# Performance work log

Hardware: AMD Instinct MI355X
Metric: run time of the kernel (lower is better)

Reference implementation:

```python
import jax, jax.numpy as jnp
import numpy as np

N_NODES = 100000
N_EDGES = 1600000
IN_FEA = 128
HIDDEN = 128
OUT_FEA = 40


def setup_inputs() -> dict:
    key = jax.random.key(0)
    k1, k2, k3, k4 = jax.random.split(key, 4)
    x = jax.random.normal(k1, (N_NODES, IN_FEA), dtype=jnp.float32)
    edge_index = jax.random.randint(k2, (2, N_EDGES), 0, N_NODES, dtype=jnp.int32)
    # Glorot-ish scaled weights
    W1 = jax.random.normal(k3, (IN_FEA, HIDDEN), dtype=jnp.float32) * (1.0 / np.sqrt(IN_FEA))
    b1 = jnp.zeros((HIDDEN,), dtype=jnp.float32)
    W2 = jax.random.normal(k4, (HIDDEN, OUT_FEA), dtype=jnp.float32) * (1.0 / np.sqrt(HIDDEN))
    b2 = jnp.zeros((OUT_FEA,), dtype=jnp.float32)
    return {"x": x, "edge_index": edge_index, "W1": W1, "b1": b1, "W2": W2, "b2": b2}


def _gcn_conv(x, src, dst, norm, W, b, n_nodes):
    # Linear transform first (PyG GCNConv order), then normalized scatter-add.
    h = x @ W                                   # [N, H]
    msg = h[src] * norm[:, None]                # [E+N, H] gather + scale
    out = jax.ops.segment_sum(msg, dst, num_segments=n_nodes)
    return out + b


def reference(x, edge_index, W1, b1, W2, b2):
    n = x.shape[0]
    loops = jnp.arange(n, dtype=edge_index.dtype)
    src = jnp.concatenate([edge_index[0], loops])  # add self-loops
    dst = jnp.concatenate([edge_index[1], loops])
    # Symmetric degree normalization: deg computed at destination (col)
    deg = jax.ops.segment_sum(jnp.ones_like(dst, dtype=x.dtype), dst, num_segments=n)
    dinv = jax.lax.rsqrt(jnp.maximum(deg, 1.0))
    norm = dinv[src] * dinv[dst]                # [E+N]

    h = jax.nn.relu(_gcn_conv(x, src, dst, norm, W1, b1, n))
    # dropout is identity in eval mode
    logits = _gcn_conv(h, src, dst, norm, W2, b2, n)
    return jax.nn.log_softmax(logits, axis=1)
```

## Files before the change

kernel.cpp:

```cpp
#include <hip/hip_runtime.h>
#include <math.h>

#define N_NODES 100000
#define N_EDGES 1600000
#define CHUNK 4096
#define NCH ((N_EDGES + CHUNK - 1) / CHUNK)
#define DSH 9
#define NBD ((N_NODES + 511) / 512)
#define CAP 9216
#define RCAP 10240

typedef __attribute__((ext_vector_type(8))) short bf16x8;
typedef __attribute__((ext_vector_type(4))) float f32x4;
typedef __attribute__((ext_vector_type(2))) float f32x2;

union U4S8 { uint4 u; bf16x8 s; };

__device__ inline unsigned pk_bf16(float a, float b) {
    unsigned ua = __float_as_uint(a), ub = __float_as_uint(b);
    ua = (ua + 0x7FFFu + ((ua >> 16) & 1u)) >> 16;
    ub = (ub + 0x7FFFu + ((ub >> 16) & 1u)) >> 16;
    return (ua & 0xFFFFu) | (ub << 16);
}
__device__ inline unsigned short bf16_1(float a) {
    unsigned ua = __float_as_uint(a);
    return (unsigned short)((ua + 0x7FFFu + ((ua >> 16) & 1u)) >> 16);
}
__device__ inline float bf_lo(unsigned u) { return __uint_as_float(u << 16); }
__device__ inline float bf_hi(unsigned u) { return __uint_as_float(u & 0xFFFF0000u); }

__device__ inline bf16x8 load_cvt8(const float* p) {
    float4 f0 = *(const float4*)p;
    float4 f1 = *(const float4*)(p + 4);
    U4S8 r;
    r.u = make_uint4(pk_bf16(f0.x, f0.y), pk_bf16(f0.z, f0.w),
                     pk_bf16(f1.x, f1.y), pk_bf16(f1.z, f1.w));
    return r.s;
}

__device__ inline void acc8_fp8(f32x2* a, uint2 v) {
    a[0] += __builtin_amdgcn_cvt_pk_f32_fp8((int)v.x, false);
    a[1] += __builtin_amdgcn_cvt_pk_f32_fp8((int)v.x, true);
    a[2] += __builtin_amdgcn_cvt_pk_f32_fp8((int)v.y, false);
    a[3] += __builtin_amdgcn_cvt_pk_f32_fp8((int)v.y, true);
}


__global__ __launch_bounds__(256) void k_prep(const float* __restrict__ W1, const float* __restrict__ W2,
                                              unsigned* __restrict__ W1t, unsigned* __restrict__ W2t,
                                              unsigned* __restrict__ Hb, unsigned* __restrict__ H2b) {
    __shared__ short L[16384];
    int t = threadIdx.x;
    if (blockIdx.x == 0) {
        for (int i = t; i < 16384; i += 256) {
            int k = i >> 7, n = i & 127;
            L[n * 128 + k] = (short)bf16_1(W1[i]);
        }
        __syncthreads();
        uint4* out = (uint4*)W1t;
        const uint4* src = (const uint4*)L;
        for (int i = t; i < 2048; i += 256) out[i] = src[i];
        if (t < 32) Hb[(size_t)N_NODES * 32 + t] = 0u;
    } else {
        for (int i = t; i < 48 * 128; i += 256) L[i] = 0;
        __syncthreads();
        for (int i = t; i < 5120; i += 256) {
            int k = i / 40, n = i - k * 40;
            L[n * 128 + k] = (short)bf16_1(W2[i]);
        }
        __syncthreads();
        uint4* out = (uint4*)W2t;
        const uint4* src = (const uint4*)L;
        for (int i = t; i < 768; i += 256) out[i] = src[i];
        if (t < 10) H2b[(size_t)N_NODES * 10 + t] = 0u;
    }
}


__global__ __launch_bounds__(256) void k_partD(const int* __restrict__ src, const int* __restrict__ dst,
                                               int* __restrict__ gtails, unsigned* __restrict__ staged, int E) {
    __shared__ int hist[NBD];
    __shared__ int tails[NBD];
    int t = threadIdx.x, c = blockIdx.x;
    if (t < NBD) hist[t] = 0;
    __syncthreads();
    int be = c * CHUNK, cw = min(CHUNK, E - be);
    for (int l = t; l < cw; l += 256) atomicAdd(&hist[dst[be + l] >> DSH], 1);
    __syncthreads();
    if (t < NBD) tails[t] = t * CAP + atomicAdd(&gtails[t], hist[t]);
    __syncthreads();
    for (int l = t; l < cw; l += 256) {
        int d = dst[be + l];
        int idx = atomicAdd(&tails[d >> DSH], 1);
        staged[idx] = ((unsigned)src[be + l] << DSH) | (unsigned)(d & 511);
    }
}

__global__ __launch_bounds__(256) void k_rank(const unsigned* __restrict__ staged, const int* __restrict__ gtails,
                                              int* __restrict__ csr, int* __restrict__ rowptr,
                                              int* __restrict__ cnt, float* __restrict__ dinv, int N) {
    __shared__ unsigned ebuf[RCAP];
    __shared__ int deg[512];
    __shared__ int sc[256];
    __shared__ int tails[512];
    int b = blockIdx.x, t = threadIdx.x;
    int n0 = b << DSH;
    int eb = b * CAP;
    int ne = gtails[b];
    deg[t] = 0; deg[t + 256] = 0;
    __syncthreads();
    bool fit = (ne <= RCAP);
    if (fit) {
        for (int l = t; l < ne; l += 256) {
            unsigned pr = staged[eb + l];
            ebuf[l] = pr;
            atomicAdd(&deg[pr & 511], 1);
        }
    } else {
        for (int l = t; l < ne; l += 256)
            atomicAdd(&deg[staged[eb + l] & 511], 1);
    }
    __syncthreads();
    int d0 = deg[2 * t], d1 = deg[2 * t + 1];
    int ts = d0 + d1;
    sc[t] = ts; __syncthreads();
    for (int o = 1; o < 256; o <<= 1) {
        int v = (t >= o) ? sc[t - o] : 0;
        __syncthreads();
        sc[t] += v;
        __syncthreads();
    }
    int excl = sc[t] - ts;
    int na = n0 + 2 * t, nb = n0 + 2 * t + 1;
    tails[2 * t] = eb + excl;
    tails[2 * t + 1] = eb + excl + d0;
    if (na < N) { rowptr[na] = eb + excl;      cnt[na] = d0; dinv[na] = rsqrtf((float)(d0 + 1)); }
    if (nb < N) { rowptr[nb] = eb + excl + d0; cnt[nb] = d1; dinv[nb] = rsqrtf((float)(d1 + 1)); }
    __syncthreads();
    if (fit) {
        for (int l = t; l < ne; l += 256) {
            unsigned pr = ebuf[l];
            int pos = atomicAdd(&tails[pr & 511], 1);
            csr[pos] = (int)(pr >> DSH);
        }
    } else {
        for (int l = t; l < ne; l += 256) {
            unsigned pr = staged[eb + l];
            int pos = atomicAdd(&tails[pr & 511], 1);
            csr[pos] = (int)(pr >> DSH);
        }
    }
}


__global__ __launch_bounds__(256) void k_gemm1(const float* __restrict__ x, const unsigned* __restrict__ W1t,
                                               const float* __restrict__ dinv, unsigned* __restrict__ Hb, int M) {
    int w = threadIdx.x >> 6, lane = threadIdx.x & 63;
    int m_base = blockIdx.x * 128 + w * 32;
    int m = lane & 15, kg = lane >> 4;
    f32x4 acc[2][8];
    #pragma unroll
    for (int i = 0; i < 2; i++)
        #pragma unroll
        for (int j = 0; j < 8; j++) acc[i][j] = (f32x4){0.f, 0.f, 0.f, 0.f};

    int r0 = min(m_base + m, M - 1);
    int r1 = min(m_base + 16 + m, M - 1);
    const float* a0p = x + (size_t)r0 * 128 + kg * 8;
    const float* a1p = x + (size_t)r1 * 128 + kg * 8;
    const uint4* bp = (const uint4*)W1t;

    #pragma unroll
    for (int ks = 0; ks < 4; ks++) {
        bf16x8 a0 = load_cvt8(a0p + ks * 32);
        bf16x8 a1 = load_cvt8(a1p + ks * 32);
        #pragma unroll
        for (int nt = 0; nt < 8; nt++) {
            U4S8 b; b.u = bp[(nt * 16 + m) * 16 + ks * 4 + kg];
            acc[0][nt] = __builtin_amdgcn_mfma_f32_16x16x32_bf16(a0, b.s, acc[0][nt], 0, 0, 0);
            acc[1][nt] = __builtin_amdgcn_mfma_f32_16x16x32_bf16(a1, b.s, acc[1][nt], 0, 0, 0);
        }
    }
    #pragma unroll
    for (int mt = 0; mt < 2; mt++) {
        #pragma unroll
        for (int r = 0; r < 4; r++) {
            int row = m_base + mt * 16 + kg * 4 + r;
            float di = dinv[min(row, M - 1)];
            bool on = (row < M) && ((m & 3) == 0);
            #pragma unroll
            for (int nt = 0; nt < 8; nt++) {
                float v = acc[mt][nt][r] * di;
                float v1 = __shfl_xor(v, 1);
                unsigned wlo = (unsigned)__builtin_amdgcn_cvt_pk_fp8_f32(v, v1, 0, false);
                unsigned whi = __shfl_xor(wlo, 2);
                unsigned u = (wlo & 0xFFFFu) | (whi << 16);
                if (on) Hb[(size_t)row * 32 + nt * 4 + (m >> 2)] = u;
            }
        }
    }
}


__global__ __launch_bounds__(256) void k_prop1(const unsigned* __restrict__ Hb, const int* __restrict__ rowptr,
                                               const int* __restrict__ cnt, const int* __restrict__ csr,
                                               const float* __restrict__ dinv, const float* __restrict__ b1,
                                               unsigned* __restrict__ h1b, int N) {
    int lane = threadIdx.x & 63;
    int g = lane >> 4, q = lane & 15;
    int i = blockIdx.x * 16 + (threadIdx.x >> 6) * 4 + g;
    if (i >= N) return;
    const uint2* H2 = (const uint2*)Hb;

    f32x2 a0[4], a1[4], a2[4], a3[4];
    #pragma unroll
    for (int k = 0; k < 4; k++) {
        a0[k] = (f32x2){0.f, 0.f}; a1[k] = (f32x2){0.f, 0.f};
        a2[k] = (f32x2){0.f, 0.f}; a3[k] = (f32x2){0.f, 0.f};
    }

    {
        uint2 sv = H2[(size_t)i * 16 + q];
        acc8_fp8(a0, sv);
    }

    int s = rowptr[i];
    int e = s + cnt[i];
    int p = s;
    for (; p + 4 <= e; p += 4) {
        int j0 = csr[p];
        int j1 = csr[p + 1];
        int j2 = csr[p + 2];
        int j3 = csr[p + 3];
        uint2 v0 = H2[(size_t)j0 * 16 + q];
        uint2 v1 = H2[(size_t)j1 * 16 + q];
        uint2 v2 = H2[(size_t)j2 * 16 + q];
        uint2 v3 = H2[(size_t)j3 * 16 + q];
        acc8_fp8(a0, v0);
        acc8_fp8(a1, v1);
        acc8_fp8(a2, v2);
        acc8_fp8(a3, v3);
    }
    for (; p < e; ++p) {
        int j = csr[p];
        uint2 v = H2[(size_t)j * 16 + q];
        acc8_fp8(a0, v);
    }
    #pragma unroll
    for (int k = 0; k < 4; k++) a0[k] = (a0[k] + a1[k]) + (a2[k] + a3[k]);

    float di = dinv[i];
    float4 bA = ((const float4*)b1)[q * 2];
    float4 bB = ((const float4*)b1)[q * 2 + 1];
    float o0 = fmaxf(di * a0[0].x + bA.x, 0.f);
    float o1 = fmaxf(di * a0[0].y + bA.y, 0.f);
    float o2 = fmaxf(di * a0[1].x + bA.z, 0.f);
    float o3 = fmaxf(di * a0[1].y + bA.w, 0.f);
    float o4 = fmaxf(di * a0[2].x + bB.x, 0.f);
    float o5 = fmaxf(di * a0[2].y + bB.y, 0.f);
    float o6 = fmaxf(di * a0[3].x + bB.z, 0.f);
    float o7 = fmaxf(di * a0[3].y + bB.w, 0.f);
    ((uint4*)h1b)[(size_t)i * 16 + q] =
        make_uint4(pk_bf16(o0, o1), pk_bf16(o2, o3), pk_bf16(o4, o5), pk_bf16(o6, o7));
}


__global__ __launch_bounds__(256) void k_gemm2(const unsigned* __restrict__ h1b, const unsigned* __restrict__ W2t,
                                               const float* __restrict__ dinv, unsigned* __restrict__ H2b, int M) {
    int w = threadIdx.x >> 6, lane = threadIdx.x & 63;
    int m_base = blockIdx.x * 128 + w * 32;
    int m = lane & 15, kg = lane >> 4;
    f32x4 acc[2][3];
    #pragma unroll
    for (int i = 0; i < 2; i++)
        #pragma unroll
        for (int j = 0; j < 3; j++) acc[i][j] = (f32x4){0.f, 0.f, 0.f, 0.f};

    int r0 = min(m_base + m, M - 1);
    int r1 = min(m_base + 16 + m, M - 1);
    const uint4* a0p = (const uint4*)h1b + (size_t)r0 * 16 + kg;
    const uint4* a1p = (const uint4*)h1b + (size_t)r1 * 16 + kg;
    const uint4* bp = (const uint4*)W2t;

    #pragma unroll
    for (int ks = 0; ks < 4; ks++) {
        U4S8 a0; a0.u = a0p[ks * 4];
        U4S8 a1; a1.u = a1p[ks * 4];
        #pragma unroll
        for (int nt = 0; nt < 3; nt++) {
            U4S8 b; b.u = bp[(nt * 16 + m) * 16 + ks * 4 + kg];
            acc[0][nt] = __builtin_amdgcn_mfma_f32_16x16x32_bf16(a0.s, b.s, acc[0][nt], 0, 0, 0);
            acc[1][nt] = __builtin_amdgcn_mfma_f32_16x16x32_bf16(a1.s, b.s, acc[1][nt], 0, 0, 0);
        }
    }
    #pragma unroll
    for (int mt = 0; mt < 2; mt++) {
        #pragma unroll
        for (int r = 0; r < 4; r++) {
            int row = m_base + mt * 16 + kg * 4 + r;
            float di = dinv[min(row, M - 1)];
            #pragma unroll
            for (int nt = 0; nt < 3; nt++) {
                float v = acc[mt][nt][r] * di;
                float v1 = __shfl_xor(v, 1);
                unsigned wlo = (unsigned)__builtin_amdgcn_cvt_pk_fp8_f32(v, v1, 0, false);
                unsigned whi = __shfl_xor(wlo, 2);
                unsigned u = (wlo & 0xFFFFu) | (whi << 16);
                unsigned u2 = __shfl_xor(u, 4);
                bool on = (row < M) && ((m & 7) == 0) && (nt < 2 || m == 0);
                if (on) ((uint2*)H2b)[(size_t)row * 5 + nt * 2 + (m >> 3)] = make_uint2(u, u2);
            }
        }
    }
}


__global__ __launch_bounds__(256) void k_prop2(const unsigned* __restrict__ H2b, const int* __restrict__ rowptr,
                                               const int* __restrict__ cnt, const int* __restrict__ csr,
                                               const float* __restrict__ dinv, const float* __restrict__ b2,
                                               float* __restrict__ out, int N) {
    int lane = threadIdx.x & 63;
    int half = lane >> 5, hl = lane & 31;
    int i = blockIdx.x * 8 + (threadIdx.x >> 6) * 2 + half;
    int g = hl / 5;
    int q = hl - g * 5;
    bool gact = g < 6;
    const uint2* H2 = (const uint2*)H2b;

    f32x2 a[4];
    #pragma unroll
    for (int k = 0; k < 4; k++) a[k] = (f32x2){0.f, 0.f};

    {
        int srow = (g == 0) ? i : N;
        uint2 sv = H2[(size_t)srow * 5 + q];
        acc8_fp8(a, sv);
    }

    int s = rowptr[i];
    int e = s + cnt[i];
    for (int p = s; p < e; p += 6) {
        int idx = p + g;
        int cidx = (idx < e) ? idx : s;
        int jl = csr[cidx];
        int j = (gact && idx < e) ? jl : N;
        uint2 v = H2[(size_t)j * 5 + q];
        acc8_fp8(a, v);
    }
    int base = half << 5;
    #pragma unroll
    for (int k = 0; k < 4; k++) {
        int s1 = base + ((hl + 15) & 31);
        a[k].x += __shfl(a[k].x, s1); a[k].y += __shfl(a[k].y, s1);
    }
    #pragma unroll
    for (int k = 0; k < 4; k++) {
        int s1 = base + ((hl + 5) & 31), s2 = base + ((hl + 10) & 31);
        a[k].x += __shfl(a[k].x, s1) + __shfl(a[k].x, s2);
        a[k].y += __shfl(a[k].y, s1) + __shfl(a[k].y, s2);
    }

    bool act = (g == 0);
    float di = dinv[i];
    float l[8];
    #pragma unroll
    for (int k = 0; k < 8; k++) l[k] = -INFINITY;
    if (act) {
        float4 b0 = ((const float4*)b2)[q * 2];
        float4 b1v = ((const float4*)b2)[q * 2 + 1];
        l[0] = di * a[0].x + b0.x;  l[1] = di * a[0].y + b0.y;
        l[2] = di * a[1].x + b0.z;  l[3] = di * a[1].y + b0.w;
        l[4] = di * a[2].x + b1v.x; l[5] = di * a[2].y + b1v.y;
        l[6] = di * a[3].x + b1v.z; l[7] = di * a[3].y + b1v.w;
    }
    float m = l[0];
    #pragma unroll
    for (int k = 1; k < 8; k++) m = fmaxf(m, l[k]);
    #pragma unroll
    for (int o = 4; o >= 1; o >>= 1) m = fmaxf(m, __shfl_xor(m, o));
    float sm = 0.f;
    float ex[8];
    if (act) {
        #pragma unroll
        for (int k = 0; k < 8; k++) { ex[k] = expf(l[k] - m); sm += ex[k]; }
    }
    #pragma unroll
    for (int o = 4; o >= 1; o >>= 1) sm += __shfl_xor(sm, o);
    float lse = m + logf(sm);
    if (act) {
        ((float4*)out)[(size_t)i * 10 + q * 2] = make_float4(l[0] - lse, l[1] - lse, l[2] - lse, l[3] - lse);
        ((float4*)out)[(size_t)i * 10 + q * 2 + 1] = make_float4(l[4] - lse, l[5] - lse, l[6] - lse, l[7] - lse);
    }
}


extern "C" void kernel_launch(void* const* d_in, const int* in_sizes, int n_in,
                              void* d_out, int out_size, void* d_ws, size_t ws_size,
                              hipStream_t stream) {
    const float* x  = (const float*)d_in[0];
    const int*   ei = (const int*)d_in[1];
    const float* W1 = (const float*)d_in[2];
    const float* b1 = (const float*)d_in[3];
    const float* W2 = (const float*)d_in[4];
    const float* b2 = (const float*)d_in[5];
    float* out = (float*)d_out;
    char* ws = (char*)d_ws;
    const int N = N_NODES, E = N_EDGES;

    size_t o = 0;
    auto alloc = [&](size_t bytes) { size_t cur = o; o += (bytes + 511) & ~(size_t)511; return cur; };
    int*       cnt    = (int*)(ws + alloc((size_t)N * 4));
    int*       rowptr = (int*)(ws + alloc((size_t)N * 4));
    float*     dinv   = (float*)(ws + alloc((size_t)N * 4));
    int*       gtails = (int*)(ws + alloc((size_t)NBD * 4));
    unsigned*  staged = (unsigned*)(ws + alloc((size_t)NBD * CAP * 4));
    int*       csr    = (int*)(ws + alloc((size_t)NBD * CAP * 4));
    unsigned*  W1t    = (unsigned*)(ws + alloc(128 * 128 * 2));
    unsigned*  W2t    = (unsigned*)(ws + alloc(48 * 128 * 2));
    unsigned*  Hb     = (unsigned*)(ws + alloc((size_t)(N + 1) * 32 * 4));
    unsigned*  h1b    = (unsigned*)(ws + alloc((size_t)N * 64 * 4));
    unsigned*  H2b    = (unsigned*)(ws + alloc((size_t)(N + 1) * 10 * 4));

    const int* src = ei;
    const int* dst = ei + E;

    hipMemsetAsync(gtails, 0, (size_t)NBD * 4, stream);
    k_prep <<<2, 256, 0, stream>>>(W1, W2, W1t, W2t, Hb, H2b);
    k_partD<<<NCH, 256, 0, stream>>>(src, dst, gtails, staged, E);
    k_rank <<<NBD, 256, 0, stream>>>(staged, gtails, csr, rowptr, cnt, dinv, N);

    k_gemm1<<<(N + 127) / 128, 256, 0, stream>>>(x, W1t, dinv, Hb, N);
    k_prop1<<<(N + 15) / 16, 256, 0, stream>>>(Hb, rowptr, cnt, csr, dinv, b1, h1b, N);
    k_gemm2<<<(N + 127) / 128, 256, 0, stream>>>(h1b, W2t, dinv, H2b, N);
    k_prop2<<<(N + 7) / 8, 256, 0, stream>>>(H2b, rowptr, cnt, csr, dinv, b2, out, N);

    (void)in_sizes; (void)n_in; (void)out_size; (void)ws_size;
}
```

Measured before the change: 268.3 us.

## Halve GEMM row tiles, prefetch A operands, remap prop2 to one node per 5-lane group

Both GEMM kernels now compute 16 rows per wave instead of 32, doubling the grid, and load all A-operand data up front before the MFMA loop so the loads are in flight together. The second propagation kernel is reorganised so each 5-lane group owns a whole node and walks its edge list serially, with 4-way unrolled independent gathers and accumulators. This replaces the old scheme of splitting one node's edges across six groups and then reducing with shuffles. The aim is more parallelism and memory-level overlap and fewer cross-lane reductions. The cost is 4 idle lanes per wave in prop2, load imbalance across nodes with different degrees, and less B-operand reuse per wave in the GEMMs.

```diff
diff --git a/kernel.cpp b/kernel.cpp
--- a/kernel.cpp
+++ b/kernel.cpp
@@ -25,17 +25,6 @@
 __device__ inline unsigned short bf16_1(float a) {
     unsigned ua = __float_as_uint(a);
     return (unsigned short)((ua + 0x7FFFu + ((ua >> 16) & 1u)) >> 16);
-}
-__device__ inline float bf_lo(unsigned u) { return __uint_as_float(u << 16); }
-__device__ inline float bf_hi(unsigned u) { return __uint_as_float(u & 0xFFFF0000u); }
-
-__device__ inline bf16x8 load_cvt8(const float* p) {
-    float4 f0 = *(const float4*)p;
-    float4 f1 = *(const float4*)(p + 4);
-    U4S8 r;
-    r.u = make_uint4(pk_bf16(f0.x, f0.y), pk_bf16(f0.z, f0.w),
-                     pk_bf16(f1.x, f1.y), pk_bf16(f1.z, f1.w));
-    return r.s;
 }
 
 __device__ inline void acc8_fp8(f32x2* a, uint2 v) {
@@ -155,48 +144,49 @@
 
 __global__ __launch_bounds__(256) void k_gemm1(const float* __restrict__ x, const unsigned* __restrict__ W1t,
                                                const float* __restrict__ dinv, unsigned* __restrict__ Hb, int M) {
-    int w = threadIdx.x >> 6, lane = threadIdx.x & 63;
-    int m_base = blockIdx.x * 128 + w * 32;
+    int t = threadIdx.x;
+    int w = t >> 6, lane = t & 63;
+    int m_base = blockIdx.x * 64 + w * 16;
     int m = lane & 15, kg = lane >> 4;
-    f32x4 acc[2][8];
-    #pragma unroll
-    for (int i = 0; i < 2; i++)
-        #pragma unroll
-        for (int j = 0; j < 8; j++) acc[i][j] = (f32x4){0.f, 0.f, 0.f, 0.f};
 
     int r0 = min(m_base + m, M - 1);
-    int r1 = min(m_base + 16 + m, M - 1);
     const float* a0p = x + (size_t)r0 * 128 + kg * 8;
-    const float* a1p = x + (size_t)r1 * 128 + kg * 8;
+
+    float4 fa[4][2];
+    #pragma unroll
+    for (int ks = 0; ks < 4; ks++) {
+        fa[ks][0] = *(const float4*)(a0p + ks * 32);
+        fa[ks][1] = *(const float4*)(a0p + ks * 32 + 4);
+    }
+
+    f32x4 acc[8];
+    #pragma unroll
+    for (int j = 0; j < 8; j++) acc[j] = (f32x4){0.f, 0.f, 0.f, 0.f};
+
     const uint4* bp = (const uint4*)W1t;
-
     #pragma unroll
     for (int ks = 0; ks < 4; ks++) {
-        bf16x8 a0 = load_cvt8(a0p + ks * 32);
-        bf16x8 a1 = load_cvt8(a1p + ks * 32);
+        U4S8 a0; a0.u = make_uint4(pk_bf16(fa[ks][0].x, fa[ks][0].y), pk_bf16(fa[ks][0].z, fa[ks][0].w),
+                                   pk_bf16(fa[ks][1].x, fa[ks][1].y), pk_bf16(fa[ks][1].z, fa[ks][1].w));
         #pragma unroll
         for (int nt = 0; nt < 8; nt++) {
             U4S8 b; b.u = bp[(nt * 16 + m) * 16 + ks * 4 + kg];
-            acc[0][nt] = __builtin_amdgcn_mfma_f32_16x16x32_bf16(a0, b.s, acc[0][nt], 0, 0, 0);
-            acc[1][nt] = __builtin_amdgcn_mfma_f32_16x16x32_bf16(a1, b.s, acc[1][nt], 0, 0, 0);
-        }
-    }
-    #pragma unroll
-    for (int mt = 0; mt < 2; mt++) {
+            acc[nt] = __builtin_amdgcn_mfma_f32_16x16x32_bf16(a0.s, b.s, acc[nt], 0, 0, 0);
+        }
+    }
+    #pragma unroll
+    for (int r = 0; r < 4; r++) {
+        int row = m_base + kg * 4 + r;
+        float di = dinv[min(row, M - 1)];
+        bool on = (row < M) && ((m & 3) == 0);
         #pragma unroll
-        for (int r = 0; r < 4; r++) {
-            int row = m_base + mt * 16 + kg * 4 + r;
-            float di = dinv[min(row, M - 1)];
-            bool on = (row < M) && ((m & 3) == 0);
-            #pragma unroll
-            for (int nt = 0; nt < 8; nt++) {
-                float v = acc[mt][nt][r] * di;
-                float v1 = __shfl_xor(v, 1);
-                unsigned wlo = (unsigned)__builtin_amdgcn_cvt_pk_fp8_f32(v, v1, 0, false);
-                unsigned whi = __shfl_xor(wlo, 2);
-                unsigned u = (wlo & 0xFFFFu) | (whi << 16);
-                if (on) Hb[(size_t)row * 32 + nt * 4 + (m >> 2)] = u;
-            }
+        for (int nt = 0; nt < 8; nt++) {
+            float v = acc[nt][r] * di;
+            float v1 = __shfl_xor(v, 1);
+            unsigned wlo = (unsigned)__builtin_amdgcn_cvt_pk_fp8_f32(v, v1, 0, false);
+            unsigned whi = __shfl_xor(wlo, 2);
+            unsigned u = (wlo & 0xFFFFu) | (whi << 16);
+            if (on) Hb[(size_t)row * 32 + nt * 4 + (m >> 2)] = u;
         }
     }
 }
@@ -267,49 +257,46 @@
 
 __global__ __launch_bounds__(256) void k_gemm2(const unsigned* __restrict__ h1b, const unsigned* __restrict__ W2t,
                                                const float* __restrict__ dinv, unsigned* __restrict__ H2b, int M) {
-    int w = threadIdx.x >> 6, lane = threadIdx.x & 63;
-    int m_base = blockIdx.x * 128 + w * 32;
+    int t = threadIdx.x;
+    int w = t >> 6, lane = t & 63;
+    int m_base = blockIdx.x * 64 + w * 16;
     int m = lane & 15, kg = lane >> 4;
-    f32x4 acc[2][3];
-    #pragma unroll
-    for (int i = 0; i < 2; i++)
-        #pragma unroll
-        for (int j = 0; j < 3; j++) acc[i][j] = (f32x4){0.f, 0.f, 0.f, 0.f};
 
     int r0 = min(m_base + m, M - 1);
-    int r1 = min(m_base + 16 + m, M - 1);
     const uint4* a0p = (const uint4*)h1b + (size_t)r0 * 16 + kg;
-    const uint4* a1p = (const uint4*)h1b + (size_t)r1 * 16 + kg;
+
+    uint4 ua0[4];
+    #pragma unroll
+    for (int ks = 0; ks < 4; ks++) ua0[ks] = a0p[ks * 4];
+
+    f32x4 acc[3];
+    #pragma unroll
+    for (int j = 0; j < 3; j++) acc[j] = (f32x4){0.f, 0.f, 0.f, 0.f};
+
     const uint4* bp = (const uint4*)W2t;
-
     #pragma unroll
     for (int ks = 0; ks < 4; ks++) {
-        U4S8 a0; a0.u = a0p[ks * 4];
-        U4S8 a1; a1.u = a1p[ks * 4];
+        U4S8 a0; a0.u = ua0[ks];
         #pragma unroll
         for (int nt = 0; nt < 3; nt++) {
             U4S8 b; b.u = bp[(nt * 16 + m) * 16 + ks * 4 + kg];
-            acc[0][nt] = __builtin_amdgcn_mfma_f32_16x16x32_bf16(a0.s, b.s, acc[0][nt], 0, 0, 0);
-            acc[1][nt] = __builtin_amdgcn_mfma_f32_16x16x32_bf16(a1.s, b.s, acc[1][nt], 0, 0, 0);
-        }
-    }
-    #pragma unroll
-    for (int mt = 0; mt < 2; mt++) {
+            acc[nt] = __builtin_amdgcn_mfma_f32_16x16x32_bf16(a0.s, b.s, acc[nt], 0, 0, 0);
+        }
+    }
+    #pragma unroll
+    for (int r = 0; r < 4; r++) {
+        int row = m_base + kg * 4 + r;
+        float di = dinv[min(row, M - 1)];
         #pragma unroll
-        for (int r = 0; r < 4; r++) {
-            int row = m_base + mt * 16 + kg * 4 + r;
-            float di = dinv[min(row, M - 1)];
-            #pragma unroll
-            for (int nt = 0; nt < 3; nt++) {
-                float v = acc[mt][nt][r] * di;
-                float v1 = __shfl_xor(v, 1);
-                unsigned wlo = (unsigned)__builtin_amdgcn_cvt_pk_fp8_f32(v, v1, 0, false);
-                unsigned whi = __shfl_xor(wlo, 2);
-                unsigned u = (wlo & 0xFFFFu) | (whi << 16);
-                unsigned u2 = __shfl_xor(u, 4);
-                bool on = (row < M) && ((m & 7) == 0) && (nt < 2 || m == 0);
-                if (on) ((uint2*)H2b)[(size_t)row * 5 + nt * 2 + (m >> 3)] = make_uint2(u, u2);
-            }
+        for (int nt = 0; nt < 3; nt++) {
+            float v = acc[nt][r] * di;
+            float v1 = __shfl_xor(v, 1);
+            unsigned wlo = (unsigned)__builtin_amdgcn_cvt_pk_fp8_f32(v, v1, 0, false);
+            unsigned whi = __shfl_xor(wlo, 2);
+            unsigned u = (wlo & 0xFFFFu) | (whi << 16);
+            unsigned u2 = __shfl_xor(u, 4);
+            bool on = (row < M) && ((m & 7) == 0) && (nt < 2 || m == 0);
+            if (on) ((uint2*)H2b)[(size_t)row * 5 + nt * 2 + (m >> 3)] = make_uint2(u, u2);
         }
     }
 }
@@ -320,77 +307,76 @@
                                                const float* __restrict__ dinv, const float* __restrict__ b2,
                                                float* __restrict__ out, int N) {
     int lane = threadIdx.x & 63;
-    int half = lane >> 5, hl = lane & 31;
-    int i = blockIdx.x * 8 + (threadIdx.x >> 6) * 2 + half;
-    int g = hl / 5;
-    int q = hl - g * 5;
-    bool gact = g < 6;
+    int wv = threadIdx.x >> 6;
+    int grp = lane / 5;
+    int q = lane - grp * 5;
+    if (grp >= 12) return;
+    int i = blockIdx.x * 48 + wv * 12 + grp;
+    if (i >= N) return;
     const uint2* H2 = (const uint2*)H2b;
 
-    f32x2 a[4];
-    #pragma unroll
-    for (int k = 0; k < 4; k++) a[k] = (f32x2){0.f, 0.f};
-
-    {
-        int srow = (g == 0) ? i : N;
-        uint2 sv = H2[(size_t)srow * 5 + q];
-        acc8_fp8(a, sv);
-    }
+    f32x2 a0[4], a1[4], a2[4], a3[4];
+    #pragma unroll
+    for (int k = 0; k < 4; k++) {
+        a0[k] = (f32x2){0.f, 0.f}; a1[k] = (f32x2){0.f, 0.f};
+        a2[k] = (f32x2){0.f, 0.f}; a3[k] = (f32x2){0.f, 0.f};
+    }
+
+    acc8_fp8(a0, H2[(size_t)i * 5 + q]);
 
     int s = rowptr[i];
     int e = s + cnt[i];
-    for (int p = s; p < e; p += 6) {
-        int idx = p + g;
-        int cidx = (idx < e) ? idx : s;
-        int jl = csr[cidx];
-        int j = (gact && idx < e) ? jl : N;
-        uint2 v = H2[(size_t)j * 5 + q];
-        acc8_fp8(a, v);
-    }
-    int base = half << 5;
-    #pragma unroll
-    for (int k = 0; k < 4; k++) {
-        int s1 = base + ((hl + 15) & 31);
-        a[k].x += __shfl(a[k].x, s1); a[k].y += __shfl(a[k].y, s1);
-    }
-    #pragma unroll
-    for (int k = 0; k < 4; k++) {
-        int s1 = base + ((hl + 5) & 31), s2 = base + ((hl + 10) & 31);
-        a[k].x += __shfl(a[k].x, s1) + __shfl(a[k].x, s2);
-        a[k].y += __shfl(a[k].y, s1) + __shfl(a[k].y, s2);
-    }
-
-    bool act = (g == 0);
+    int p = s;
+    for (; p + 4 <= e; p += 4) {
+        int j0 = csr[p];
+        int j1 = csr[p + 1];
+        int j2 = csr[p + 2];
+        int j3 = csr[p + 3];
+        uint2 v0 = H2[(size_t)j0 * 5 + q];
+        uint2 v1 = H2[(size_t)j1 * 5 + q];
+        uint2 v2 = H2[(size_t)j2 * 5 + q];
+        uint2 v3 = H2[(size_t)j3 * 5 + q];
+        acc8_fp8(a0, v0);
+        acc8_fp8(a1, v1);
+        acc8_fp8(a2, v2);
+        acc8_fp8(a3, v3);
+    }
+    for (; p < e; ++p) {
+        uint2 v = H2[(size_t)csr[p] * 5 + q];
+        acc8_fp8(a0, v);
+    }
+    #pragma unroll
+    for (int k = 0; k < 4; k++) a0[k] = (a0[k] + a1[k]) + (a2[k] + a3[k]);
+
     float di = dinv[i];
+    float4 b0 = ((const float4*)b2)[q * 2];
+    float4 b1v = ((const float4*)b2)[q * 2 + 1];
     float l[8];
-    #pragma unroll
-    for (int k = 0; k < 8; k++) l[k] = -INFINITY;
-    if (act) {
-        float4 b0 = ((const float4*)b2)[q * 2];
-        float4 b1v = ((const float4*)b2)[q * 2 + 1];
-        l[0] = di * a[0].x + b0.x;  l[1] = di * a[0].y + b0.y;
-        l[2] = di * a[1].x + b0.z;  l[3] = di * a[1].y + b0.w;
-        l[4] = di * a[2].x + b1v.x; l[5] = di * a[2].y + b1v.y;
-        l[6] = di * a[3].x + b1v.z; l[7] = di * a[3].y + b1v.w;
-    }
-    float m = l[0];
-    #pragma unroll
-    for (int k = 1; k < 8; k++) m = fmaxf(m, l[k]);
-    #pragma unroll
-    for (int o = 4; o >= 1; o >>= 1) m = fmaxf(m, __shfl_xor(m, o));
+    l[0] = di * a0[0].x + b0.x;  l[1] = di * a0[0].y + b0.y;
+    l[2] = di * a0[1].x + b0.z;  l[3] = di * a0[1].y + b0.w;
+    l[4] = di * a0[2].x + b1v.x; l[5] = di * a0[2].y + b1v.y;
+    l[6] = di * a0[3].x + b1v.z; l[7] = di * a0[3].y + b1v.w;
+
+    float mx = l[0];
+    #pragma unroll
+    for (int k = 1; k < 8; k++) mx = fmaxf(mx, l[k]);
+    int gb = grp * 5;
+    mx = fmaxf(mx, __shfl(mx, gb + (q + 1) % 5));
+    mx = fmaxf(mx, __shfl(mx, gb + (q + 2) % 5));
+    mx = fmaxf(mx, __shfl(mx, gb + (q + 4) % 5));
+
     float sm = 0.f;
-    float ex[8];
-    if (act) {
-        #pragma unroll
-        for (int k = 0; k < 8; k++) { ex[k] = expf(l[k] - m); sm += ex[k]; }
-    }
-    #pragma unroll
-    for (int o = 4; o >= 1; o >>= 1) sm += __shfl_xor(sm, o);
-    float lse = m + logf(sm);
-    if (act) {
-        ((float4*)out)[(size_t)i * 10 + q * 2] = make_float4(l[0] - lse, l[1] - lse, l[2] - lse, l[3] - lse);
-        ((float4*)out)[(size_t)i * 10 + q * 2 + 1] = make_float4(l[4] - lse, l[5] - lse, l[6] - lse, l[7] - lse);
-    }
+    #pragma unroll
+    for (int k = 0; k < 8; k++) sm += expf(l[k] - mx);
+    float st = sm;
+    st += __shfl(sm, gb + (q + 1) % 5);
+    st += __shfl(sm, gb + (q + 2) % 5);
+    st += __shfl(sm, gb + (q + 3) % 5);
+    st += __shfl(sm, gb + (q + 4) % 5);
+    float lse = mx + logf(st);
+
+    ((float4*)out)[(size_t)i * 10 + q * 2]     = make_float4(l[0] - lse, l[1] - lse, l[2] - lse, l[3] - lse);
+    ((float4*)out)[(size_t)i * 10 + q * 2 + 1] = make_float4(l[4] - lse, l[5] - lse, l[6] - lse, l[7] - lse);
 }
 
 
@@ -429,10 +415,10 @@
     k_partD<<<NCH, 256, 0, stream>>>(src, dst, gtails, staged, E);
     k_rank <<<NBD, 256, 0, stream>>>(staged, gtails, csr, rowptr, cnt, dinv, N);
 
-    k_gemm1<<<(N + 127) / 128, 256, 0, stream>>>(x, W1t, dinv, Hb, N);
+    k_gemm1<<<(N + 63) / 64, 256, 0, stream>>>(x, W1t, dinv, Hb, N);
     k_prop1<<<(N + 15) / 16, 256, 0, stream>>>(Hb, rowptr, cnt, csr, dinv, b1, h1b, N);
-    k_gemm2<<<(N + 127) / 128, 256, 0, stream>>>(h1b, W2t, dinv, H2b, N);
-    k_prop2<<<(N + 7) / 8, 256, 0, stream>>>(H2b, rowptr, cnt, csr, dinv, b2, out, N);
+    k_gemm2<<<(N + 63) / 64, 256, 0, stream>>>(h1b, W2t, dinv, H2b, N);
+    k_prop2<<<(N + 47) / 48, 256, 0, stream>>>(H2b, rowptr, cnt, csr, dinv, b2, out, N);
 
     (void)in_sizes; (void)n_in; (void)out_size; (void)ws_size;
 }
```

After: 259.3 us. 1.04x faster.
